# Kernel optimization log

Hardware: AMD Instinct MI355X
Metric: run time of the kernel (lower is better)

Reference implementation:

```python
import jax, jax.numpy as jnp
import numpy as np

EPS = 1e-4

@jax.custom_vjp
def binarize(x):
    # BinaryConnectDeterministic: sign with sign(0)=+1
    return jnp.where(x >= 0, 1.0, -1.0).astype(x.dtype)

def _bin_fwd(x):
    return binarize(x), x

def _bin_bwd(x, g):
    # straight-through estimator, clipped to |x| <= 1
    return (g * (jnp.abs(x) <= 1).astype(g.dtype),)

binarize.defvjp(_bin_fwd, _bin_bwd)

def ap2(x):
    # approximate power-of-2: sign(x) * 2^round(log2|x|); grad is 0 a.e. (round/sign)
    a = jnp.maximum(jnp.abs(x), 1e-38)
    return jnp.sign(x) * jnp.exp2(jnp.round(jnp.log2(a)))

def shift_bn(x, gamma, beta, axes):
    # shift-based batch norm (BNN paper): var approximated via centered*AP2(centered),
    # inverse std and gamma replaced by their AP2 approximations. Training-mode batch stats.
    mean = jnp.mean(x, axis=axes, keepdims=True)
    c = x - mean
    var = jnp.mean(c * ap2(c), axis=axes, keepdims=True)
    xhat = c * ap2(1.0 / jnp.sqrt(var + EPS))
    shape = [1] * x.ndim
    shape[1] = x.shape[1]
    return ap2(gamma.reshape(shape)) * xhat + beta.reshape(shape)

def conv_bin(x, w, b):
    y = jax.lax.conv_general_dilated(x, binarize(w), (1, 1), [(1, 1), (1, 1)],
                                     dimension_numbers=('NCHW', 'OIHW', 'NCHW'))
    return y + b[None, :, None, None]

def maxpool3s2(x):
    return jax.lax.reduce_window(x, -jnp.inf, jax.lax.max,
                                 (1, 1, 3, 3), (1, 1, 2, 2), 'VALID')


def setup_inputs() -> dict:
    key = jax.random.key(0)
    ks = jax.random.split(key, 8)
    B, NU = 2048, 2048
    inp = {
        'x': jax.random.normal(ks[0], (B, 784), jnp.float32),
        'conv1_w': jax.random.normal(ks[1], (32, 1, 3, 3), jnp.float32) * 0.1,
        'conv1_b': jnp.zeros((32,), jnp.float32),
        'g1': jnp.ones((32,), jnp.float32), 'b1': jnp.zeros((32,), jnp.float32),
        'conv2_w': jax.random.normal(ks[2], (64, 32, 3, 3), jnp.float32) * 0.1,
        'conv2_b': jnp.zeros((64,), jnp.float32),
        'g2': jnp.ones((64,), jnp.float32), 'b2': jnp.zeros((64,), jnp.float32),
        'lin3_w': jax.random.normal(ks[3], (NU, 10816), jnp.float32) * 0.02,
        'lin3_b': jnp.zeros((NU,), jnp.float32),
        'g3': jnp.ones((NU,), jnp.float32), 'b3': jnp.zeros((NU,), jnp.float32),
        'lin4_w': jax.random.normal(ks[4], (10, NU), jnp.float32) * 0.02,
        'lin4_b': jnp.zeros((10,), jnp.float32),
    }
    return inp


def reference(x, conv1_w, conv1_b, g1, b1, conv2_w, conv2_b, g2, b2,
              lin3_w, lin3_b, g3, b3, lin4_w, lin4_b):
    h = x.reshape(-1, 1, 28, 28)
    h = jax.nn.relu(conv_bin(h, conv1_w, conv1_b))
    h = shift_bn(h, g1, b1, axes=(0, 2, 3))
    h = binarize(h)
    h = jax.nn.relu(conv_bin(h, conv2_w, conv2_b))
    h = maxpool3s2(h)                       # [B,64,13,13]
    h = shift_bn(h, g2, b2, axes=(0, 2, 3))
    h = binarize(h)
    h = h.reshape(h.shape[0], -1)           # [B,10816]
    h = jax.nn.relu(h @ binarize(lin3_w).T + lin3_b)
    h = shift_bn(h, g3, b3, axes=(0,))
    h = binarize(h)
    return h @ binarize(lin4_w).T + lin4_b  # [B,10] (no norm4/logsoftmax in forward)
```

## Files before the change

### kernel.cpp

```cpp
#include <hip/hip_runtime.h>

#define BB 2048
#define IMG 784
#define HWD 28
#define C1 32
#define C2 64
#define PP 169
#define PD 13
#define F3 10816
#define N3 2048
#define K4W 32
#define NOUT 10
#define CONV 27
#define PADW 30
#define OCCHUNK 8
#define OCH 32
#define SCRS 736

typedef unsigned long long u64;
typedef int v4i __attribute__((ext_vector_type(4)));

__device__ __forceinline__ float ap2mag(float c) {
    unsigned int a = __float_as_uint(c) & 0x7fffffffu;
    unsigned int e = (a >> 23) + ((a & 0x7fffffu) > 0x3504f3u);
    return __uint_as_float(e << 23);
}
__device__ __forceinline__ float ap2sgn(float g) {
    unsigned int u = __float_as_uint(g);
    unsigned int a = u & 0x7fffffffu;
    if (a == 0) return 0.f;
    unsigned int e = (a >> 23) + ((a & 0x7fffffu) > 0x3504f3u);
    return __uint_as_float((u & 0x80000000u) | (e << 23));
}

__global__ __launch_bounds__(256) void stage0(const float* __restrict__ x,
                                              const float* __restrict__ w1, const float* __restrict__ cb1,
                                              float* __restrict__ part1, float* __restrict__ w1b,
                                              const float* __restrict__ w2, unsigned int* __restrict__ w2p,
                                              const float* __restrict__ w3, char* __restrict__ wp3i,
                                              const float* __restrict__ w4, u64* __restrict__ wp4) {
    __shared__ float xs[30 * PADW];
    __shared__ float red[4 * C1];
    int n = blockIdx.x, tid = threadIdx.x;
    int lane = tid & 63, wv = tid >> 6;
    {
        int idx = n * 256 + tid;
        int nthr = gridDim.x * 256;
        int total = (N3 * F3) / 4;
        for (int t = idx; t < total; t += nthr) {
            float4 wv4 = *(const float4*)(w3 + (size_t)t * 4);
            unsigned int w = (wv4.x >= 0.f ? 0x01u : 0xffu)
                           | (wv4.y >= 0.f ? 0x01u : 0xffu) << 8
                           | (wv4.z >= 0.f ? 0x01u : 0xffu) << 16
                           | (wv4.w >= 0.f ? 0x01u : 0xffu) << 24;
            *(unsigned int*)(wp3i + (size_t)t * 4) = w;
        }
    }
    if (n == 0) {
        for (int i = tid; i < C1 * 9; i += 256) w1b[i] = (w1[i] >= 0.f) ? 1.f : -1.f;
    } else if (n == 1) {
        for (int t = tid; t < C2 * 9; t += 256) {
            int oc = t / 9, k = t % 9;
            unsigned int bits = 0;
            for (int ic = 0; ic < C1; ic++)
                bits |= (w2[oc * 288 + ic * 9 + k] >= 0.f ? 1u : 0u) << ic;
            w2p[t] = bits;
        }
    } else if (n == 2) {
        for (int w = wv; w < NOUT * K4W; w += 4) {
            int o = w / K4W, j = w % K4W;
            float wvl = w4[o * N3 + j * 64 + lane];
            u64 mask = __ballot(wvl >= 0.f);
            if (lane == 0) wp4[w] = mask;
        }
    }
    for (int i = tid; i < 30 * PADW; i += 256) {
        int r = i / PADW - 1, c = i % PADW - 1;
        float v = 0.f;
        if (r >= 0 && r < HWD && c >= 0 && c < HWD) v = x[n * IMG + r * HWD + c];
        xs[i] = v;
    }
    __syncthreads();
    bool act = tid < 196;
    int r = tid / 7, c0 = (tid % 7) * 4;
    float win[18];
#pragma unroll
    for (int k = 0; k < 18; k++) win[k] = 0.f;
    if (act) {
#pragma unroll
        for (int ry = 0; ry < 3; ry++)
#pragma unroll
            for (int cx = 0; cx < 6; cx++)
                win[ry * 6 + cx] = xs[(r + ry) * PADW + c0 + cx];
    }
#pragma unroll
    for (int ch = 0; ch < C1; ch++) {
        float a = 0.f;
        if (act) {
            float k0 = (w1[ch * 9 + 0] >= 0.f) ? 1.f : -1.f, k1 = (w1[ch * 9 + 1] >= 0.f) ? 1.f : -1.f;
            float k2 = (w1[ch * 9 + 2] >= 0.f) ? 1.f : -1.f, k3 = (w1[ch * 9 + 3] >= 0.f) ? 1.f : -1.f;
            float k4 = (w1[ch * 9 + 4] >= 0.f) ? 1.f : -1.f, k5 = (w1[ch * 9 + 5] >= 0.f) ? 1.f : -1.f;
            float k6 = (w1[ch * 9 + 6] >= 0.f) ? 1.f : -1.f, k7 = (w1[ch * 9 + 7] >= 0.f) ? 1.f : -1.f;
            float k8 = (w1[ch * 9 + 8] >= 0.f) ? 1.f : -1.f;
            float b = cb1[ch];
#pragma unroll
            for (int px = 0; px < 4; px++) {
                float s = win[px] * k0 + win[px + 1] * k1 + win[px + 2] * k2
                        + win[6 + px] * k3 + win[7 + px] * k4 + win[8 + px] * k5
                        + win[12 + px] * k6 + win[13 + px] * k7 + win[14 + px] * k8;
                a += fmaxf(s + b, 0.f);
            }
        }
        for (int off = 32; off; off >>= 1) a += __shfl_down(a, off);
        if (lane == 0) red[wv * C1 + ch] = a;
    }
    __syncthreads();
    if (tid < C1) part1[n * C1 + tid] = red[tid] + red[C1 + tid] + red[2 * C1 + tid] + red[3 * C1 + tid];
}

__global__ __launch_bounds__(256) void conv1_var(const float* __restrict__ x,
                            const float* __restrict__ w1b,
                            const float* __restrict__ cb1, const float* __restrict__ mean1,
                            float* __restrict__ part) {
    __shared__ float xs[30 * PADW];
    __shared__ float red[4 * C1];
    int n = blockIdx.x, tid = threadIdx.x;
    for (int i = tid; i < 30 * PADW; i += 256) {
        int r = i / PADW - 1, c = i % PADW - 1;
        float v = 0.f;
        if (r >= 0 && r < HWD && c >= 0 && c < HWD) v = x[n * IMG + r * HWD + c];
        xs[i] = v;
    }
    __syncthreads();
    bool act = tid < 196;
    int r = tid / 7, c0 = (tid % 7) * 4;
    float win[18];
#pragma unroll
    for (int k = 0; k < 18; k++) win[k] = 0.f;
    if (act) {
#pragma unroll
        for (int ry = 0; ry < 3; ry++)
#pragma unroll
            for (int cx = 0; cx < 6; cx++)
                win[ry * 6 + cx] = xs[(r + ry) * PADW + c0 + cx];
    }
    int lane = tid & 63, wv = tid >> 6;
#pragma unroll
    for (int ch = 0; ch < C1; ch++) {
        float a = 0.f;
        if (act) {
            float k0 = w1b[ch * 9 + 0], k1 = w1b[ch * 9 + 1], k2 = w1b[ch * 9 + 2];
            float k3 = w1b[ch * 9 + 3], k4 = w1b[ch * 9 + 4], k5 = w1b[ch * 9 + 5];
            float k6 = w1b[ch * 9 + 6], k7 = w1b[ch * 9 + 7], k8 = w1b[ch * 9 + 8];
            float b = cb1[ch], m = mean1[ch];
#pragma unroll
            for (int px = 0; px < 4; px++) {
                float s = win[px] * k0 + win[px + 1] * k1 + win[px + 2] * k2
                        + win[6 + px] * k3 + win[7 + px] * k4 + win[8 + px] * k5
                        + win[12 + px] * k6 + win[13 + px] * k7 + win[14 + px] * k8;
                float v = fmaxf(s + b, 0.f);
                float c = v - m;
                a += fabsf(c) * ap2mag(c);
            }
        }
        for (int off = 32; off; off >>= 1) a += __shfl_down(a, off);
        if (lane == 0) red[wv * C1 + ch] = a;
    }
    __syncthreads();
    if (tid < C1) part[n * C1 + tid] = red[tid] + red[C1 + tid] + red[2 * C1 + tid] + red[3 * C1 + tid];
}

__global__ __launch_bounds__(256) void conv1_pack(const float* __restrict__ x,
                           const float* __restrict__ w1b,
                           const float* __restrict__ cb1, const float* __restrict__ mean1,
                           const float* __restrict__ scale1, const float* __restrict__ beta1,
                           unsigned int* __restrict__ s1p) {
    __shared__ float xs[30 * PADW];
    int n = blockIdx.x, tid = threadIdx.x;
    for (int i = tid; i < 30 * PADW; i += 256) {
        int r = i / PADW - 1, c = i % PADW - 1;
        float v = 0.f;
        if (r >= 0 && r < HWD && c >= 0 && c < HWD) v = x[n * IMG + r * HWD + c];
        xs[i] = v;
    }
    __syncthreads();
    if (tid >= 196) return;
    int r = tid / 7, c0 = (tid % 7) * 4;
    float win[18];
#pragma unroll
    for (int ry = 0; ry < 3; ry++)
#pragma unroll
        for (int cx = 0; cx < 6; cx++)
            win[ry * 6 + cx] = xs[(r + ry) * PADW + c0 + cx];
    unsigned int bits0 = 0, bits1 = 0, bits2 = 0, bits3 = 0;
#pragma unroll
    for (int ch = 0; ch < C1; ch++) {
        float k0 = w1b[ch * 9 + 0], k1 = w1b[ch * 9 + 1], k2 = w1b[ch * 9 + 2];
        float k3 = w1b[ch * 9 + 3], k4 = w1b[ch * 9 + 4], k5 = w1b[ch * 9 + 5];
        float k6 = w1b[ch * 9 + 6], k7 = w1b[ch * 9 + 7], k8 = w1b[ch * 9 + 8];
        float b = cb1[ch], m = mean1[ch], sc = scale1[ch], bt = beta1[ch];
#pragma unroll
        for (int px = 0; px < 4; px++) {
            float s = win[px] * k0 + win[px + 1] * k1 + win[px + 2] * k2
                    + win[6 + px] * k3 + win[7 + px] * k4 + win[8 + px] * k5
                    + win[12 + px] * k6 + win[13 + px] * k7 + win[14 + px] * k8;
            float v = fmaxf(s + b, 0.f);
            float val = sc * (v - m) + bt;
            unsigned int bit = (val >= 0.f ? 1u : 0u) << ch;
            if (px == 0) bits0 |= bit;
            else if (px == 1) bits1 |= bit;
            else if (px == 2) bits2 |= bit;
            else bits3 |= bit;
        }
    }
    uint4 w4v = make_uint4(bits0, bits1, bits2, bits3);
    *reinterpret_cast<uint4*>(&s1p[n * IMG + r * HWD + c0]) = w4v;
}

__global__ __launch_bounds__(256) void conv2pool(const unsigned int* __restrict__ s1p,
                                                 const unsigned int* __restrict__ w2p,
                                                 const float* __restrict__ cb2,
                                                 short* __restrict__ p2i,
                                                 float* __restrict__ part2) {
    __shared__ unsigned int spad[29 * PADW];
    __shared__ short scr[OCCHUNK * SCRS];
    __shared__ float psum[OCCHUNK * PP];
    __shared__ float pm[OCH];
    int n = blockIdx.x, ocb = blockIdx.y * OCH, tid = threadIdx.x;
    for (int i = tid; i < 29 * PADW; i += 256) {
        int r = i / PADW, c = i - r * PADW;
        unsigned int v = 0;
        if (r >= 1 && c >= 1 && c <= 28) v = s1p[n * IMG + (r - 1) * HWD + (c - 1)];
        spad[i] = v;
    }
    __syncthreads();
    unsigned int win[3][9];
    bool top_[3], left_[3];
    bool act2 = (tid + 512) < CONV * CONV;
#pragma unroll
    for (int pi = 0; pi < 3; pi++) {
        int p = tid + pi * 256;
        if (p >= CONV * CONV) p = 0;
        int y = p / CONV, xx = p - y * CONV;
        top_[pi] = (y == 0);
        left_[pi] = (xx == 0);
        const unsigned int* bp = &spad[y * PADW + xx];
#pragma unroll
        for (int ky = 0; ky < 3; ky++)
#pragma unroll
            for (int kx = 0; kx < 3; kx++)
                win[pi][ky * 3 + kx] = bp[ky * PADW + kx];
    }
    int lane = tid & 63, wv = tid >> 6;
    for (int base = 0; base < OCH; base += OCCHUNK) {
        for (int ol = 0; ol < OCCHUNK; ol++) {
            int oc = ocb + base + ol;
            unsigned int w0 = w2p[oc * 9 + 0], w1 = w2p[oc * 9 + 1], w2 = w2p[oc * 9 + 2];
            unsigned int w3 = w2p[oc * 9 + 3], w4 = w2p[oc * 9 + 4], w5 = w2p[oc * 9 + 5];
            unsigned int w6 = w2p[oc * 9 + 6], w7 = w2p[oc * 9 + 7], w8 = w2p[oc * 9 + 8];
            int p0 = __popc(w0), p1 = __popc(w1), p2 = __popc(w2);
            int p3 = __popc(w3), p6 = __popc(w6);
            int ct = 192 + 2 * (p0 + p1 + p2);
            int cl = 192 + 2 * (p0 + p3 + p6);
            int cc = 128 + 2 * (p0 + p1 + p2 + p3 + p6);
#pragma unroll
            for (int pi = 0; pi < 3; pi++) {
                int s = __popc(win[pi][0] ^ w0) + __popc(win[pi][1] ^ w1) + __popc(win[pi][2] ^ w2)
                      + __popc(win[pi][3] ^ w3) + __popc(win[pi][4] ^ w4) + __popc(win[pi][5] ^ w5)
                      + __popc(win[pi][6] ^ w6) + __popc(win[pi][7] ^ w7) + __popc(win[pi][8] ^ w8);
                int off = top_[pi] ? (left_[pi] ? cc : ct) : (left_[pi] ? cl : 288);
                if (pi < 2 || act2) scr[ol * SCRS + tid + pi * 256] = (short)(off - 2 * s);
            }
        }
        __syncthreads();
        for (int q = tid; q < OCCHUNK * PP; q += 256) {
            int ol = q / PP, pix = q - ol * PP;
            int py = pix / PD, px = pix - py * PD;
            const short* rr = &scr[ol * SCRS + (2 * py) * CONV + 2 * px];
            int m0 = max(max((int)rr[0], (int)rr[1]), (int)rr[2]);
            int m1 = max(max((int)rr[CONV], (int)rr[CONV + 1]), (int)rr[CONV + 2]);
            int m2 = max(max((int)rr[2 * CONV], (int)rr[2 * CONV + 1]), (int)rr[2 * CONV + 2]);
            int val = max(max(m0, m1), m2);
            p2i[n * F3 + (ocb + base + ol) * PP + pix] = (short)val;
            psum[q] = fmaxf((float)val + cb2[ocb + base + ol], 0.f);
        }
        __syncthreads();
        for (int ol = wv; ol < OCCHUNK; ol += 4) {
            float a = 0.f;
            for (int p = lane; p < PP; p += 64) a += psum[ol * PP + p];
            for (int off = 32; off; off >>= 1) a += __shfl_down(a, off);
            if (lane == 0) pm[base + ol] = a;
        }
        __syncthreads();
    }
    if (tid < OCH) part2[n * C2 + ocb + tid] = pm[tid];
}

__global__ __launch_bounds__(256) void p2_var(const short* __restrict__ p2i,
                         const float* __restrict__ cb2,
                         const float* __restrict__ mean2, float* __restrict__ part) {
    int n = blockIdx.x, tid = threadIdx.x, lane = tid & 63, wv = tid >> 6;
    const short* rowb = p2i + (size_t)n * F3;
    __shared__ float red[C2];
#pragma unroll
    for (int i = 0; i < 16; i++) {
        int ch = wv * 16 + i;
        const short* row = rowb + ch * PP;
        float b = cb2[ch];
        float m = mean2[ch];
        float a = 0.f;
        for (int p = lane; p < PP; p += 64) {
            float v = fmaxf((float)row[p] + b, 0.f);
            float c = v - m;
            a += fabsf(c) * ap2mag(c);
        }
        for (int off = 32; off; off >>= 1) a += __shfl_down(a, off);
        if (lane == 0) red[ch] = a;
    }
    __syncthreads();
    if (tid < C2) part[n * C2 + tid] = red[tid];
}

__global__ __launch_bounds__(256) void reduce_stats(const float* __restrict__ part, int nch, int nblk,
                             const float* __restrict__ g, float* __restrict__ outv,
                             int mode, double count) {
    int ch = blockIdx.x, tid = threadIdx.x;
    double a = 0.0;
    for (int i = tid; i < nblk; i += 256) a += (double)part[(size_t)i * nch + ch];
    __shared__ double red[4];
    for (int off = 32; off; off >>= 1) a += __shfl_down(a, off);
    int lane = tid & 63, wv = tid >> 6;
    if (lane == 0) red[wv] = a;
    __syncthreads();
    if (tid == 0) {
        double s = red[0] + red[1] + red[2] + red[3];
        if (mode == 0) {
            outv[ch] = (float)(s / count);
        } else {
            float var = (float)(s / count);
            float inv = 1.0f / sqrtf(var + 1e-4f);
            outv[ch] = ap2sgn(g[ch]) * ap2mag(inv);
        }
    }
}

__global__ __launch_bounds__(256) void p2_packi8(const short* __restrict__ p2i, const float* __restrict__ cb2,
                        const float* __restrict__ mean2, const float* __restrict__ scale2,
                        const float* __restrict__ beta2, char* __restrict__ hp3i) {
    int idx = blockIdx.x * 256 + threadIdx.x;
    int nthr = gridDim.x * 256;
    int total = (BB * F3) / 4;
    for (int t = idx; t < total; t += nthr) {
        int base = t * 4;
        int f0 = base % F3;
        unsigned int w = 0;
#pragma unroll
        for (int e = 0; e < 4; e++) {
            int f = f0 + e;
            int oc = f / PP;
            float v = fmaxf((float)p2i[base + e] + cb2[oc], 0.f);
            float val = scale2[oc] * (v - mean2[oc]) + beta2[oc];
            w |= (val >= 0.f ? 0x01u : 0xffu) << (8 * e);
        }
        *(unsigned int*)(hp3i + base) = w;
    }
}

__global__ __launch_bounds__(256) void lin3_mfma(const char* __restrict__ hp3i,
                                                 const char* __restrict__ wp3i,
                                                 const float* __restrict__ b3l,
                                                 float* __restrict__ h3,
                                                 float* __restrict__ part3) {
    __shared__ v4i aL[2][512];
    __shared__ v4i bL[2][256];
    __shared__ float csr[4][32];
    int tid = threadIdx.x;
    int lane = tid & 63, wv = tid >> 6;
    int wr = wv >> 1, wc = wv & 1;
    int m0 = blockIdx.y * 128, n0 = blockIdx.x * 64;
    int ra = tid >> 1, ha = tid & 1;
    const char* ag = hp3i + (size_t)(m0 + ra) * F3 + ha * 32;
    int abase = (ra >> 4) * 64 + (2 * ha) * 16 + (ra & 15);
    int rb = tid >> 2, qb = tid & 3;
    const char* bg = wp3i + (size_t)(n0 + rb) * F3 + qb * 16;
    int bbase = (rb >> 4) * 64 + qb * 16 + (rb & 15);
    v4i acc[4][2];
#pragma unroll
    for (int i = 0; i < 4; i++)
#pragma unroll
        for (int j = 0; j < 2; j++) acc[i][j] = (v4i){0, 0, 0, 0};
    v4i a0 = *(const v4i*)ag, a1 = *(const v4i*)(ag + 16);
    v4i b0 = *(const v4i*)bg;
    aL[0][abase] = a0; aL[0][abase + 16] = a1;
    bL[0][bbase] = b0;
    __syncthreads();
    for (int c = 0; c < 169; c++) {
        int cur = c & 1, nxt = cur ^ 1;
        if (c < 168) {
            ag += 64; bg += 64;
            a0 = *(const v4i*)ag; a1 = *(const v4i*)(ag + 16);
            b0 = *(const v4i*)bg;
        }
        v4i af[4], bf[2];
#pragma unroll
        for (int i = 0; i < 4; i++) af[i] = aL[cur][(wr * 4 + i) * 64 + lane];
#pragma unroll
        for (int j = 0; j < 2; j++) bf[j] = bL[cur][(wc * 2 + j) * 64 + lane];
#pragma unroll
        for (int i = 0; i < 4; i++)
#pragma unroll
            for (int j = 0; j < 2; j++)
                acc[i][j] = __builtin_amdgcn_mfma_i32_16x16x64_i8(af[i], bf[j], acc[i][j], 0, 0, 0);
        if (c < 168) {
            aL[nxt][abase] = a0; aL[nxt][abase + 16] = a1;
            bL[nxt][bbase] = b0;
        }
        __syncthreads();
    }
    int q = lane >> 4, m16 = lane & 15;
    float cs[2] = {0.f, 0.f};
#pragma unroll
    for (int j = 0; j < 2; j++) {
        int col = n0 + wc * 32 + j * 16 + m16;
        float bias = b3l[col];
#pragma unroll
        for (int i = 0; i < 4; i++) {
            int rowb = m0 + wr * 64 + i * 16 + q * 4;
#pragma unroll
            for (int rg = 0; rg < 4; rg++) {
                float v = fmaxf((float)acc[i][j][rg] + bias, 0.f);
                h3[(size_t)(rowb + rg) * N3 + col] = v;
                cs[j] += v;
            }
        }
    }
#pragma unroll
    for (int j = 0; j < 2; j++) {
        cs[j] += __shfl_xor(cs[j], 16);
        cs[j] += __shfl_xor(cs[j], 32);
        if (lane < 16) csr[wv][j * 16 + m16] = cs[j];
    }
    __syncthreads();
    if (tid < 64) {
        int wcc = tid >> 5, cc = tid & 31;
        part3[(size_t)blockIdx.y * N3 + n0 + tid] = csr[wcc][cc] + csr[2 + wcc][cc];
    }
}

__global__ __launch_bounds__(256) void h3_finish(const float* __restrict__ h3,
                                                 const float* __restrict__ part3,
                                                 const float* __restrict__ g3,
                                                 float* __restrict__ mean3, float* __restrict__ scale3) {
    int nn = blockIdx.x, tid = threadIdx.x;
    __shared__ float msh;
    __shared__ double redd[4];
    if (tid < 64) {
        float a = (tid < 16) ? part3[(size_t)tid * N3 + nn] : 0.f;
        for (int off = 8; off; off >>= 1) a += __shfl_down(a, off);
        if (tid == 0) { float m = a / (float)BB; mean3[nn] = m; msh = m; }
    }
    __syncthreads();
    float m = msh;
    float acc = 0.f;
#pragma unroll
    for (int q = 0; q < 8; q++) {
        float v = h3[(size_t)(q * 256 + tid) * N3 + nn];
        float c = v - m;
        acc += fabsf(c) * ap2mag(c);
    }
    double a = (double)acc;
    for (int off = 32; off; off >>= 1) a += __shfl_down(a, off);
    int lane = tid & 63, wv = tid >> 6;
    if (lane == 0) redd[wv] = a;
    __syncthreads();
    if (tid == 0) {
        float var = (float)((redd[0] + redd[1] + redd[2] + redd[3]) / (double)BB);
        float inv = 1.0f / sqrtf(var + 1e-4f);
        scale3[nn] = ap2sgn(g3[nn]) * ap2mag(inv);
    }
}

__global__ __launch_bounds__(256) void h4_out(const float* __restrict__ h3,
                                              const float* __restrict__ mean3, const float* __restrict__ scale3,
                                              const float* __restrict__ bt3,
                                              const u64* __restrict__ wp4, const float* __restrict__ b4,
                                              float* __restrict__ out) {
    __shared__ u64 hb[K4W];
    __shared__ u64 wsh[NOUT * 33];
    int m = blockIdx.x, tid = threadIdx.x, lane = tid & 63, wv = tid >> 6;
    for (int i = tid; i < NOUT * K4W; i += 256) wsh[(i / K4W) * 33 + (i % K4W)] = wp4[i];
#pragma unroll
    for (int q = 0; q < 8; q++) {
        int j = wv * 8 + q;
        int f = j * 64 + lane;
        float v = h3[(size_t)m * N3 + f];
        float val = scale3[f] * (v - mean3[f]) + bt3[f];
        u64 mask = __ballot(val >= 0.f);
        if (lane == 0) hb[j] = mask;
    }
    __syncthreads();
    if (tid < NOUT) {
        int c = 0;
#pragma unroll
        for (int k = 0; k < K4W; k++) c += (int)__popcll(hb[k] ^ wsh[tid * 33 + k]);
        out[m * NOUT + tid] = (float)(N3 - 2 * c) + b4[tid];
    }
}

extern "C" void kernel_launch(void* const* d_in, const int* in_sizes, int n_in,
                              void* d_out, int out_size, void* d_ws, size_t ws_size,
                              hipStream_t stream) {
    const float* x   = (const float*)d_in[0];
    const float* w1  = (const float*)d_in[1];
    const float* cb1 = (const float*)d_in[2];
    const float* g1  = (const float*)d_in[3];
    const float* bt1 = (const float*)d_in[4];
    const float* w2  = (const float*)d_in[5];
    const float* cb2 = (const float*)d_in[6];
    const float* g2  = (const float*)d_in[7];
    const float* bt2 = (const float*)d_in[8];
    const float* w3  = (const float*)d_in[9];
    const float* b3l = (const float*)d_in[10];
    const float* g3  = (const float*)d_in[11];
    const float* bt3 = (const float*)d_in[12];
    const float* w4  = (const float*)d_in[13];
    const float* b4l = (const float*)d_in[14];
    float* out = (float*)d_out;

    char* base = (char*)d_ws;
    size_t off = 0;
    auto carve = [&](size_t bytes) { char* p = base + off; off = (off + bytes + 255) & ~(size_t)255; return p; };
    char* bufA = carve((size_t)BB * C2 * PP * 2);
    char* bufB = carve((size_t)BB * F3);
    char* bufC = carve((size_t)N3 * F3);
    short* p2i         = (short*)bufA;
    float* h3          = (float*)bufA;
    char* hp3i         = bufB;
    unsigned int* s1p  = (unsigned int*)bufB;
    char* wp3i         = bufC;
    u64* wp4           = (u64*)carve((size_t)NOUT * K4W * 8);
    unsigned int* w2p  = (unsigned int*)carve((size_t)C2 * 9 * 4);
    float* w1b         = (float*)carve((size_t)C1 * 9 * 4);
    float* part1       = (float*)carve((size_t)BB * C1 * 4);
    float* part2       = (float*)carve((size_t)BB * C2 * 4);
    float* part3       = (float*)carve((size_t)16 * N3 * 4);
    float* fstats      = (float*)carve((size_t)(32 + 32 + 64 + 64 + 2048 + 2048) * 4);
    float* mean1 = fstats;          float* scale1 = fstats + 32;
    float* mean2 = fstats + 64;     float* scale2 = fstats + 128;
    float* mean3 = fstats + 192;    float* scale3 = fstats + 2240;

    stage0<<<BB, 256, 0, stream>>>(x, w1, cb1, part1, w1b, w2, w2p, w3, wp3i, w4, wp4);
    reduce_stats<<<C1, 256, 0, stream>>>(part1, C1, BB, g1, mean1, 0, (double)BB * IMG);
    conv1_var<<<BB, 256, 0, stream>>>(x, w1b, cb1, mean1, part1);
    reduce_stats<<<C1, 256, 0, stream>>>(part1, C1, BB, g1, scale1, 1, (double)BB * IMG);
    conv1_pack<<<BB, 256, 0, stream>>>(x, w1b, cb1, mean1, scale1, bt1, s1p);
    conv2pool<<<dim3(BB, 2), 256, 0, stream>>>(s1p, w2p, cb2, p2i, part2);
    reduce_stats<<<C2, 256, 0, stream>>>(part2, C2, BB, g2, mean2, 0, (double)BB * PP);
    p2_var<<<BB, 256, 0, stream>>>(p2i, cb2, mean2, part2);
    reduce_stats<<<C2, 256, 0, stream>>>(part2, C2, BB, g2, scale2, 1, (double)BB * PP);
    p2_packi8<<<2048, 256, 0, stream>>>(p2i, cb2, mean2, scale2, bt2, hp3i);
    lin3_mfma<<<dim3(32, 16), 256, 0, stream>>>(hp3i, wp3i, b3l, h3, part3);
    h3_finish<<<N3, 256, 0, stream>>>(h3, part3, g3, mean3, scale3);
    h4_out<<<BB, 256, 0, stream>>>(h3, mean3, scale3, bt3, wp4, b4l, out);

    (void)in_sizes; (void)n_in; (void)out_size; (void)ws_size;
}
```

Measured before the change: 584.6 us.

## Compute binary conv2 with int8 MFMA instead of XOR-popcount

Conv2 is recast as an implicit GEMM. The bit-packed activations are expanded to ±1 int8 in shared memory, the weights are pre-laid out as ±1 int8 fragments, and the kernel uses mfma_i32_32x32x32_i8 over the 9 taps. Zero padding is handled by zero bytes, so the border popcount corrections go away. Each block now covers all 64 output channels in two halves instead of splitting channels across two blocks, so the activation tile is staged once per image. Shared memory use rises (about 27KB image plus 47KB scratch), which may reduce occupancy.

After: 580.0 us. Within noise of the previous version (-0.8%).

```diff
diff --git a/kernel.cpp b/kernel.cpp
--- a/kernel.cpp
+++ b/kernel.cpp
@@ -14,11 +14,12 @@
 #define CONV 27
 #define PADW 30
 #define OCCHUNK 8
-#define OCH 32
-#define SCRS 736
+#define IMGC 29
+#define SCRP 740
 
 typedef unsigned long long u64;
 typedef int v4i __attribute__((ext_vector_type(4)));
+typedef int v16i __attribute__((ext_vector_type(16)));
 
 __device__ __forceinline__ float ap2mag(float c) {
     unsigned int a = __float_as_uint(c) & 0x7fffffffu;
@@ -36,7 +37,7 @@
 __global__ __launch_bounds__(256) void stage0(const float* __restrict__ x,
                                               const float* __restrict__ w1, const float* __restrict__ cb1,
                                               float* __restrict__ part1, float* __restrict__ w1b,
-                                              const float* __restrict__ w2, unsigned int* __restrict__ w2p,
+                                              const float* __restrict__ w2, char* __restrict__ w2i8,
                                               const float* __restrict__ w3, char* __restrict__ wp3i,
                                               const float* __restrict__ w4, u64* __restrict__ wp4) {
     __shared__ float xs[30 * PADW];
@@ -59,12 +60,15 @@
     if (n == 0) {
         for (int i = tid; i < C1 * 9; i += 256) w1b[i] = (w1[i] >= 0.f) ? 1.f : -1.f;
     } else if (n == 1) {
-        for (int t = tid; t < C2 * 9; t += 256) {
-            int oc = t / 9, k = t % 9;
-            unsigned int bits = 0;
-            for (int ic = 0; ic < C1; ic++)
-                bits |= (w2[oc * 288 + ic * 9 + k] >= 0.f ? 1u : 0u) << ic;
-            w2p[t] = bits;
+        for (int i = tid; i < 2 * 9 * 64 * 16; i += 256) {
+            int hf = i / 9216;
+            int r = i - hf * 9216;
+            int t = r >> 10;
+            int l = (r >> 4) & 63;
+            int j = i & 15;
+            int oc = hf * 32 + (l & 31);
+            int ic = ((l >> 5) << 4) + j;
+            w2i8[i] = (w2[oc * 288 + ic * 9 + t] >= 0.f) ? (char)1 : (char)(-1);
         }
     } else if (n == 2) {
         for (int w = wv; w < NOUT * K4W; w += 4) {
@@ -218,82 +222,106 @@
 }
 
 __global__ __launch_bounds__(256) void conv2pool(const unsigned int* __restrict__ s1p,
-                                                 const unsigned int* __restrict__ w2p,
+                                                 const char* __restrict__ w2i8,
                                                  const float* __restrict__ cb2,
                                                  short* __restrict__ p2i,
                                                  float* __restrict__ part2) {
-    __shared__ unsigned int spad[29 * PADW];
-    __shared__ short scr[OCCHUNK * SCRS];
+    __shared__ char img[IMGC * IMGC * 32];
+    __shared__ short scr[32 * SCRP];
     __shared__ float psum[OCCHUNK * PP];
-    __shared__ float pm[OCH];
-    int n = blockIdx.x, ocb = blockIdx.y * OCH, tid = threadIdx.x;
-    for (int i = tid; i < 29 * PADW; i += 256) {
-        int r = i / PADW, c = i - r * PADW;
-        unsigned int v = 0;
-        if (r >= 1 && c >= 1 && c <= 28) v = s1p[n * IMG + (r - 1) * HWD + (c - 1)];
-        spad[i] = v;
-    }
-    __syncthreads();
-    unsigned int win[3][9];
-    bool top_[3], left_[3];
-    bool act2 = (tid + 512) < CONV * CONV;
-#pragma unroll
-    for (int pi = 0; pi < 3; pi++) {
-        int p = tid + pi * 256;
-        if (p >= CONV * CONV) p = 0;
-        int y = p / CONV, xx = p - y * CONV;
-        top_[pi] = (y == 0);
-        left_[pi] = (xx == 0);
-        const unsigned int* bp = &spad[y * PADW + xx];
-#pragma unroll
-        for (int ky = 0; ky < 3; ky++)
-#pragma unroll
-            for (int kx = 0; kx < 3; kx++)
-                win[pi][ky * 3 + kx] = bp[ky * PADW + kx];
-    }
+    __shared__ float pm[C2];
+    int n = blockIdx.x, tid = threadIdx.x;
     int lane = tid & 63, wv = tid >> 6;
-    for (int base = 0; base < OCH; base += OCCHUNK) {
-        for (int ol = 0; ol < OCCHUNK; ol++) {
-            int oc = ocb + base + ol;
-            unsigned int w0 = w2p[oc * 9 + 0], w1 = w2p[oc * 9 + 1], w2 = w2p[oc * 9 + 2];
-            unsigned int w3 = w2p[oc * 9 + 3], w4 = w2p[oc * 9 + 4], w5 = w2p[oc * 9 + 5];
-            unsigned int w6 = w2p[oc * 9 + 6], w7 = w2p[oc * 9 + 7], w8 = w2p[oc * 9 + 8];
-            int p0 = __popc(w0), p1 = __popc(w1), p2 = __popc(w2);
-            int p3 = __popc(w3), p6 = __popc(w6);
-            int ct = 192 + 2 * (p0 + p1 + p2);
-            int cl = 192 + 2 * (p0 + p3 + p6);
-            int cc = 128 + 2 * (p0 + p1 + p2 + p3 + p6);
-#pragma unroll
-            for (int pi = 0; pi < 3; pi++) {
-                int s = __popc(win[pi][0] ^ w0) + __popc(win[pi][1] ^ w1) + __popc(win[pi][2] ^ w2)
-                      + __popc(win[pi][3] ^ w3) + __popc(win[pi][4] ^ w4) + __popc(win[pi][5] ^ w5)
-                      + __popc(win[pi][6] ^ w6) + __popc(win[pi][7] ^ w7) + __popc(win[pi][8] ^ w8);
-                int off = top_[pi] ? (left_[pi] ? cc : ct) : (left_[pi] ? cl : 288);
-                if (pi < 2 || act2) scr[ol * SCRS + tid + pi * 256] = (short)(off - 2 * s);
+    for (int i = tid; i < IMGC * IMGC; i += 256) {
+        int r = i / IMGC, c = i - r * IMGC;
+        unsigned int w = 0u;
+        if (r >= 1 && c >= 1) w = s1p[n * IMG + (r - 1) * HWD + (c - 1)];
+        unsigned int d[8];
+        if (r == 0 || c == 0) {
+#pragma unroll
+            for (int e = 0; e < 8; e++) d[e] = 0u;
+        } else {
+#pragma unroll
+            for (int e = 0; e < 8; e++) {
+                unsigned int nib = (w >> (4 * e)) & 0xFu;
+                unsigned int t = (nib & 1u) | ((nib & 2u) << 7) | ((nib & 4u) << 14) | ((nib & 8u) << 21);
+                d[e] = 0xFFFFFFFFu - t * 0xFEu;
+            }
+        }
+        *(uint4*)&img[i * 32] = make_uint4(d[0], d[1], d[2], d[3]);
+        *(uint4*)&img[i * 32 + 16] = make_uint4(d[4], d[5], d[6], d[7]);
+    }
+    __syncthreads();
+    int hh = lane >> 5;
+    int l31 = lane & 31;
+    for (int hf = 0; hf < 2; hf++) {
+        v4i bf[9];
+#pragma unroll
+        for (int t = 0; t < 9; t++)
+            bf[t] = *(const v4i*)(w2i8 + (hf * 9 + t) * 1024 + lane * 16);
+#pragma unroll
+        for (int j = 0; j < 3; j++) {
+            int mtA = wv + 8 * j, mtB = mtA + 4;
+            int pA = mtA * 32 + l31; if (pA > 728) pA = 728;
+            int pB = mtB * 32 + l31; if (pB > 728) pB = 728;
+            int yA = pA / 27, xA = pA - yA * 27;
+            int yB = pB / 27, xB = pB - yB * 27;
+            int aA = (yA * IMGC + xA) * 32 + hh * 16;
+            int aB = (yB * IMGC + xB) * 32 + hh * 16;
+            v16i accA = {0,0,0,0,0,0,0,0,0,0,0,0,0,0,0,0};
+            v16i accB = {0,0,0,0,0,0,0,0,0,0,0,0,0,0,0,0};
+#pragma unroll
+            for (int ky = 0; ky < 3; ky++)
+#pragma unroll
+                for (int kx = 0; kx < 3; kx++) {
+                    v4i fA = *(const v4i*)&img[aA + (ky * IMGC + kx) * 32];
+                    v4i fB = *(const v4i*)&img[aB + (ky * IMGC + kx) * 32];
+                    accA = __builtin_amdgcn_mfma_i32_32x32x32_i8(fA, bf[ky * 3 + kx], accA, 0, 0, 0);
+                    accB = __builtin_amdgcn_mfma_i32_32x32x32_i8(fB, bf[ky * 3 + kx], accB, 0, 0, 0);
+                }
+            short* sr = &scr[l31 * SCRP];
+#pragma unroll
+            for (int g = 0; g < 4; g++) {
+                short4 sA;
+                sA.x = (short)accA[4 * g + 0]; sA.y = (short)accA[4 * g + 1];
+                sA.z = (short)accA[4 * g + 2]; sA.w = (short)accA[4 * g + 3];
+                *(short4*)&sr[mtA * 32 + g * 8 + 4 * hh] = sA;
+            }
+            if (mtB < 23) {
+#pragma unroll
+                for (int g = 0; g < 4; g++) {
+                    short4 sB;
+                    sB.x = (short)accB[4 * g + 0]; sB.y = (short)accB[4 * g + 1];
+                    sB.z = (short)accB[4 * g + 2]; sB.w = (short)accB[4 * g + 3];
+                    *(short4*)&sr[mtB * 32 + g * 8 + 4 * hh] = sB;
+                }
             }
         }
         __syncthreads();
-        for (int q = tid; q < OCCHUNK * PP; q += 256) {
-            int ol = q / PP, pix = q - ol * PP;
-            int py = pix / PD, px = pix - py * PD;
-            const short* rr = &scr[ol * SCRS + (2 * py) * CONV + 2 * px];
-            int m0 = max(max((int)rr[0], (int)rr[1]), (int)rr[2]);
-            int m1 = max(max((int)rr[CONV], (int)rr[CONV + 1]), (int)rr[CONV + 2]);
-            int m2 = max(max((int)rr[2 * CONV], (int)rr[2 * CONV + 1]), (int)rr[2 * CONV + 2]);
-            int val = max(max(m0, m1), m2);
-            p2i[n * F3 + (ocb + base + ol) * PP + pix] = (short)val;
-            psum[q] = fmaxf((float)val + cb2[ocb + base + ol], 0.f);
-        }
-        __syncthreads();
-        for (int ol = wv; ol < OCCHUNK; ol += 4) {
-            float a = 0.f;
-            for (int p = lane; p < PP; p += 64) a += psum[ol * PP + p];
-            for (int off = 32; off; off >>= 1) a += __shfl_down(a, off);
-            if (lane == 0) pm[base + ol] = a;
-        }
-        __syncthreads();
-    }
-    if (tid < OCH) part2[n * C2 + ocb + tid] = pm[tid];
+        for (int base = 0; base < 32; base += OCCHUNK) {
+            for (int q = tid; q < OCCHUNK * PP; q += 256) {
+                int ol = q / PP, pix = q - ol * PP;
+                int py = pix / PD, px = pix - py * PD;
+                const short* rr = &scr[(base + ol) * SCRP + (2 * py) * CONV + 2 * px];
+                int m0 = max(max((int)rr[0], (int)rr[1]), (int)rr[2]);
+                int m1 = max(max((int)rr[CONV], (int)rr[CONV + 1]), (int)rr[CONV + 2]);
+                int m2 = max(max((int)rr[2 * CONV], (int)rr[2 * CONV + 1]), (int)rr[2 * CONV + 2]);
+                int val = max(max(m0, m1), m2);
+                int oc = hf * 32 + base + ol;
+                p2i[n * F3 + oc * PP + pix] = (short)val;
+                psum[q] = fmaxf((float)val + cb2[oc], 0.f);
+            }
+            __syncthreads();
+            for (int ol = wv; ol < OCCHUNK; ol += 4) {
+                float a = 0.f;
+                for (int pp = lane; pp < PP; pp += 64) a += psum[ol * PP + pp];
+                for (int off = 32; off; off >>= 1) a += __shfl_down(a, off);
+                if (lane == 0) pm[hf * 32 + base + ol] = a;
+            }
+            __syncthreads();
+        }
+    }
+    if (tid < C2) part2[n * C2 + tid] = pm[tid];
 }
 
 __global__ __launch_bounds__(256) void p2_var(const short* __restrict__ p2i,
@@ -539,7 +567,7 @@
     unsigned int* s1p  = (unsigned int*)bufB;
     char* wp3i         = bufC;
     u64* wp4           = (u64*)carve((size_t)NOUT * K4W * 8);
-    unsigned int* w2p  = (unsigned int*)carve((size_t)C2 * 9 * 4);
+    char* w2i8         = (char*)carve((size_t)2 * 9 * 64 * 16);
     float* w1b         = (float*)carve((size_t)C1 * 9 * 4);
     float* part1       = (float*)carve((size_t)BB * C1 * 4);
     float* part2       = (float*)carve((size_t)BB * C2 * 4);
@@ -549,12 +577,12 @@
     float* mean2 = fstats + 64;     float* scale2 = fstats + 128;
     float* mean3 = fstats + 192;    float* scale3 = fstats + 2240;
 
-    stage0<<<BB, 256, 0, stream>>>(x, w1, cb1, part1, w1b, w2, w2p, w3, wp3i, w4, wp4);
+    stage0<<<BB, 256, 0, stream>>>(x, w1, cb1, part1, w1b, w2, w2i8, w3, wp3i, w4, wp4);
     reduce_stats<<<C1, 256, 0, stream>>>(part1, C1, BB, g1, mean1, 0, (double)BB * IMG);
     conv1_var<<<BB, 256, 0, stream>>>(x, w1b, cb1, mean1, part1);
     reduce_stats<<<C1, 256, 0, stream>>>(part1, C1, BB, g1, scale1, 1, (double)BB * IMG);
     conv1_pack<<<BB, 256, 0, stream>>>(x, w1b, cb1, mean1, scale1, bt1, s1p);
-    conv2pool<<<dim3(BB, 2), 256, 0, stream>>>(s1p, w2p, cb2, p2i, part2);
+    conv2pool<<<BB, 256, 0, stream>>>(s1p, w2i8, cb2, p2i, part2);
     reduce_stats<<<C2, 256, 0, stream>>>(part2, C2, BB, g2, mean2, 0, (double)BB * PP);
     p2_var<<<BB, 256, 0, stream>>>(p2i, cb2, mean2, part2);
     reduce_stats<<<C2, 256, 0, stream>>>(part2, C2, BB, g2, scale2, 1, (double)BB * PP);
```
